# Optimization experiments

Measured on AMD Instinct MI355X. Metric: run time of the kernel, lower is better.

Reference implementation:

```python
import jax, jax.numpy as jnp
import numpy as np

K = 32          # init k
E = 0.003       # EMA rate e


def setup_inputs() -> dict:
    key = jax.random.key(0)
    k1, _ = jax.random.split(key)
    features = jax.random.normal(k1, (512, 6, 8192), dtype=jnp.float32)
    threshold = jnp.zeros((1,), dtype=jnp.float32)
    return {"features": features, "threshold": threshold}


def reference(features, threshold):
    batch_size, n_layers, d_features = features.shape
    batch_k = K * batch_size * n_layers
    flat = features.reshape(-1)                      # [B*L*D]
    topk_vals, topk_idxs = jax.lax.top_k(flat, batch_k)
    topk_vals = jax.nn.relu(topk_vals)
    out = jnp.zeros_like(flat).at[topk_idxs].set(topk_vals)
    out = out.reshape(batch_size, n_layers, d_features)
    min_k = jax.lax.stop_gradient(jnp.min(topk_vals))
    new_threshold = (1.0 - E) * threshold + E * min_k
    return out, new_threshold
```

## Files before the change

kernel.cpp:

```cpp
#include <hip/hip_runtime.h>
#include <stdint.h>

#define K_TOTAL   98304u
#define EMA_RATE  0.003f

#define SBINS      16384
#define SBIN_SHIFT 18
#define SAMPLE_VEC 131072
#define STARGET    8192u
#define P2_BINS    4096
#define P2_SHIFT   12
#define LCAP       1024
#define CAP2       65536u
#define EQCAP      256

#define MP_BLOCKS  3072
#define MP_UNROLL  8

__device__ __forceinline__ unsigned f2key(float x) {
    unsigned u = __float_as_uint(x);
    return (u & 0x80000000u) ? ~u : (u | 0x80000000u);
}
__device__ __forceinline__ float key2f(unsigned key) {
    unsigned u = (key & 0x80000000u) ? (key & 0x7FFFFFFFu) : ~key;
    return __uint_as_float(u);
}

__global__ __launch_bounds__(256) void sample_hist_kernel(
        const float4* __restrict__ in, unsigned* __restrict__ shist) {
    __shared__ unsigned h[SBINS];
    for (int i = threadIdx.x; i < SBINS; i += 256) h[i] = 0;
    __syncthreads();
    unsigned tid = blockIdx.x * 256 + threadIdx.x;
    unsigned nth = gridDim.x * 256;
    float4 v[4];
    #pragma unroll
    for (int u = 0; u < 4; ++u) {
        unsigned j = tid + u * nth;
        v[u] = (j < SAMPLE_VEC) ? in[j] : make_float4(0.f, 0.f, 0.f, 0.f);
    }
    #pragma unroll
    for (int u = 0; u < 4; ++u) {
        unsigned j = tid + u * nth;
        if (j < SAMPLE_VEC) {
            atomicAdd(&h[f2key(v[u].x) >> SBIN_SHIFT], 1u);
            atomicAdd(&h[f2key(v[u].y) >> SBIN_SHIFT], 1u);
            atomicAdd(&h[f2key(v[u].z) >> SBIN_SHIFT], 1u);
            atomicAdd(&h[f2key(v[u].w) >> SBIN_SHIFT], 1u);
        }
    }
    __syncthreads();
    for (int i = threadIdx.x; i < SBINS; i += 256) {
        unsigned c = h[i];
        if (c) atomicAdd(&shist[i], c);
    }
}

__global__ __launch_bounds__(1024) void sample_scan_kernel(
        const unsigned* __restrict__ shist, unsigned* __restrict__ res) {
    __shared__ unsigned psum[1024];
    const int T = 1024;
    const int GB = SBINS / T;
    int t = threadIdx.x;
    int hi = SBINS - 1 - t * GB;
    unsigned c[GB];
    #pragma unroll
    for (int j = 0; j < GB; ++j) c[j] = shist[hi - j];
    unsigned s = 0;
    #pragma unroll
    for (int j = 0; j < GB; ++j) s += c[j];
    psum[t] = s;
    __syncthreads();
    for (int off = 1; off < T; off <<= 1) {
        unsigned o = (t >= off) ? psum[t - off] : 0u;
        __syncthreads();
        psum[t] += o;
        __syncthreads();
    }
    unsigned cum = psum[t] - s;
    for (int j = 0; j < GB; ++j) {
        if (cum < STARGET && cum + c[j] >= STARGET) {
            unsigned bin = (unsigned)(hi - j);
            unsigned bb = (bin > 0) ? bin - 1 : 0;
            res[0] = bb << SBIN_SHIFT;
        }
        cum += c[j];
    }
}

__global__ __launch_bounds__(256) void main_pass_kernel(
        const float4* __restrict__ in, const unsigned* __restrict__ res,
        float* __restrict__ cval, unsigned* __restrict__ cidx,
        unsigned* __restrict__ gcnt, unsigned cap, int nvec) {
    __shared__ float    lval[LCAP];
    __shared__ unsigned lidx[LCAP];
    __shared__ unsigned lcnt, lbase;
    if (threadIdx.x == 0) lcnt = 0;
    __syncthreads();
    unsigned base = res[0];
    unsigned tid = blockIdx.x * 256 + threadIdx.x;
    unsigned nth = gridDim.x * 256;
    for (unsigned i0 = tid; i0 < (unsigned)nvec; i0 += MP_UNROLL * nth) {
        float4 v[MP_UNROLL];
        #pragma unroll
        for (int u = 0; u < MP_UNROLL; ++u) {
            unsigned j = i0 + u * nth;
            v[u] = (j < (unsigned)nvec) ? in[j]
                   : make_float4(-1e30f, -1e30f, -1e30f, -1e30f);
        }
        #pragma unroll
        for (int u = 0; u < MP_UNROLL; ++u) {
            unsigned j = i0 + u * nth;
            unsigned idx = 4u * j;
            float xs[4] = {v[u].x, v[u].y, v[u].z, v[u].w};
            #pragma unroll
            for (int c = 0; c < 4; ++c) {
                unsigned key = f2key(xs[c]);
                if (key >= base) {
                    unsigned p = atomicAdd(&lcnt, 1u);
                    if (p < LCAP) { lval[p] = xs[c]; lidx[p] = idx + c; }
                    else {
                        unsigned q = atomicAdd(gcnt, 1u);
                        if (q < cap) { cval[q] = xs[c]; cidx[q] = idx + c; }
                    }
                }
            }
        }
    }
    __syncthreads();
    unsigned n = min(lcnt, (unsigned)LCAP);
    if (threadIdx.x == 0) lbase = atomicAdd(gcnt, n);
    __syncthreads();
    for (unsigned j = threadIdx.x; j < n; j += 256) {
        unsigned p = lbase + j;
        if (p < cap) { cval[p] = lval[j]; cidx[p] = lidx[j]; }
    }
}

__global__ __launch_bounds__(256) void cand_hist_kernel(
        const float* __restrict__ cval, const unsigned* __restrict__ gcnt,
        const unsigned* __restrict__ res, unsigned* __restrict__ ghist,
        unsigned cap) {
    __shared__ unsigned h[P2_BINS];
    for (int i = threadIdx.x; i < P2_BINS; i += 256) h[i] = 0;
    __syncthreads();
    unsigned nc = min(*gcnt, cap);
    unsigned base = res[0];
    unsigned tid = blockIdx.x * 256 + threadIdx.x;
    unsigned nth = gridDim.x * 256;
    for (unsigned i0 = tid; i0 < nc; i0 += 4 * nth) {
        float v[4];
        #pragma unroll
        for (int u = 0; u < 4; ++u) {
            unsigned j = i0 + u * nth;
            v[u] = (j < nc) ? cval[j] : -1e30f;
        }
        #pragma unroll
        for (int u = 0; u < 4; ++u) {
            unsigned j = i0 + u * nth;
            if (j < nc) {
                unsigned g = (f2key(v[u]) - base) >> P2_SHIFT;
                if (g > P2_BINS - 1) g = P2_BINS - 1;
                atomicAdd(&h[g], 1u);
            }
        }
    }
    __syncthreads();
    for (int i = threadIdx.x; i < P2_BINS; i += 256) {
        unsigned c = h[i];
        if (c) atomicAdd(&ghist[i], c);
    }
}

__global__ __launch_bounds__(1024) void find_g_kernel(
        const unsigned* __restrict__ ghist, unsigned* __restrict__ res2) {
    __shared__ unsigned psum[1024];
    const int T = 1024;
    const int GB = P2_BINS / T;
    int t = threadIdx.x;
    int hi = P2_BINS - 1 - t * GB;
    unsigned c[GB];
    #pragma unroll
    for (int j = 0; j < GB; ++j) c[j] = ghist[hi - j];
    unsigned s = 0;
    #pragma unroll
    for (int j = 0; j < GB; ++j) s += c[j];
    psum[t] = s;
    __syncthreads();
    for (int off = 1; off < T; off <<= 1) {
        unsigned o = (t >= off) ? psum[t - off] : 0u;
        __syncthreads();
        psum[t] += o;
        __syncthreads();
    }
    unsigned cum = psum[t] - s;
    for (int j = 0; j < GB; ++j) {
        if (cum < K_TOTAL && cum + c[j] >= K_TOTAL) {
            res2[0] = (unsigned)(hi - j);
            res2[1] = K_TOTAL - cum;
        }
        cum += c[j];
    }
}

__global__ __launch_bounds__(256) void scatter_kernel(
        const float* __restrict__ cval, const unsigned* __restrict__ cidx,
        const unsigned* __restrict__ gcnt, const unsigned* __restrict__ res,
        const unsigned* __restrict__ res2,
        float* __restrict__ cval2, unsigned* __restrict__ cidx2,
        unsigned* __restrict__ cnt2, unsigned cap,
        float* __restrict__ out) {
    unsigned nc = min(*gcnt, cap);
    unsigned base = res[0];
    unsigned gstar = res2[0];
    unsigned tid = blockIdx.x * 256 + threadIdx.x;
    unsigned nth = gridDim.x * 256;
    for (unsigned i0 = tid; i0 < nc; i0 += 4 * nth) {
        float v[4];
        #pragma unroll
        for (int u = 0; u < 4; ++u) {
            unsigned j = i0 + u * nth;
            v[u] = (j < nc) ? cval[j] : -1e30f;
        }
        #pragma unroll
        for (int u = 0; u < 4; ++u) {
            unsigned j = i0 + u * nth;
            if (j < nc) {
                unsigned g = (f2key(v[u]) - base) >> P2_SHIFT;
                if (g > P2_BINS - 1) g = P2_BINS - 1;
                if (g > gstar) {
                    out[cidx[j]] = fmaxf(v[u], 0.0f);
                } else if (g == gstar) {
                    unsigned p = atomicAdd(cnt2, 1u);
                    if (p < CAP2) { cval2[p] = v[u]; cidx2[p] = cidx[j]; }
                }
            }
        }
    }
}

__global__ __launch_bounds__(256) void final_kernel(
        const float* __restrict__ cval2, const unsigned* __restrict__ cidx2,
        const unsigned* __restrict__ cnt2,
        const unsigned* __restrict__ res, const unsigned* __restrict__ res2,
        float* __restrict__ out,
        const float* __restrict__ thr_in, float* __restrict__ thr_out) {
    __shared__ unsigned h[1 << P2_SHIFT];
    __shared__ unsigned psum[256];
    __shared__ unsigned eqidx[EQCAP];
    __shared__ unsigned eqcnt;
    __shared__ unsigned sh_low, sh_need3;
    const int NB = 1 << P2_SHIFT;
    int t = threadIdx.x;
    unsigned nc2   = min(*cnt2, CAP2);
    unsigned base3 = res[0] + (res2[0] << P2_SHIFT);
    unsigned need2 = res2[1];

    for (int i = t; i < NB; i += 256) h[i] = 0;
    if (t == 0) eqcnt = 0;
    __syncthreads();
    for (unsigned i = t; i < nc2; i += 256) {
        unsigned low = f2key(cval2[i]) - base3;
        if (low > (unsigned)(NB - 1)) low = NB - 1;
        atomicAdd(&h[low], 1u);
    }
    __syncthreads();

    const int GB = NB / 256;
    int hi = NB - 1 - t * GB;
    unsigned s = 0;
    for (int j = 0; j < GB; ++j) s += h[hi - j];
    psum[t] = s;
    __syncthreads();
    for (int off = 1; off < 256; off <<= 1) {
        unsigned o = (t >= off) ? psum[t - off] : 0u;
        __syncthreads();
        psum[t] += o;
        __syncthreads();
    }
    unsigned cum = psum[t] - s;
    for (int j = 0; j < GB; ++j) {
        unsigned c = h[hi - j];
        if (cum < need2 && cum + c >= need2) {
            sh_low = (unsigned)(hi - j);
            sh_need3 = need2 - cum;
        }
        cum += c;
    }
    __syncthreads();
    unsigned kth_key = base3 + sh_low;
    unsigned need3   = sh_need3;

    for (unsigned i = t; i < nc2; i += 256) {
        float x = cval2[i];
        unsigned key = f2key(x);
        if (key > kth_key) {
            out[cidx2[i]] = fmaxf(x, 0.0f);
        } else if (key == kth_key) {
            unsigned p = atomicAdd(&eqcnt, 1u);
            if (p < EQCAP) eqidx[p] = cidx2[i];
        }
    }
    __syncthreads();

    unsigned ne = min(eqcnt, (unsigned)EQCAP);
    float vv = key2f(kth_key);
    for (unsigned e = t; e < ne; e += 256) {
        unsigned my = eqidx[e];
        unsigned rank = 0;
        for (unsigned f = 0; f < ne; ++f) rank += (eqidx[f] < my) ? 1u : 0u;
        if (rank < need3) out[my] = fmaxf(vv, 0.0f);
    }

    if (t == 0) {
        float mink = fmaxf(vv, 0.0f);
        thr_out[0] = (1.0f - EMA_RATE) * thr_in[0] + EMA_RATE * mink;
    }
}

extern "C" void kernel_launch(void* const* d_in, const int* in_sizes, int n_in,
                              void* d_out, int out_size, void* d_ws, size_t ws_size,
                              hipStream_t stream) {
    const float* feat   = (const float*)d_in[0];
    const float* thr_in = (const float*)d_in[1];
    float* out = (float*)d_out;
    int N    = in_sizes[0];
    int nvec = N / 4;

    uint8_t* w = (uint8_t*)d_ws;
    unsigned* shist = (unsigned*)w;
    unsigned* ghist = (unsigned*)(w + (64 << 10));
    unsigned* ctr   = (unsigned*)(w + (80 << 10));
    unsigned* gcnt  = ctr + 0;
    unsigned* cnt2  = ctr + 1;
    unsigned* res   = ctr + 4;
    unsigned* res2  = ctr + 8;

    size_t cand_off = (size_t)1 << 20;
    size_t avail    = (ws_size > cand_off + (CAP2 * 8 + 4096))
                        ? (ws_size - cand_off - CAP2 * 8 - 4096) / 8 : 0;
    unsigned cap = (unsigned)((avail < (size_t)(4u << 20)) ? avail : (size_t)(4u << 20));
    float*    cval  = (float*)(w + cand_off);
    unsigned* cidx  = (unsigned*)(w + cand_off + (size_t)cap * 4);
    float*    cval2 = (float*)(w + cand_off + (size_t)cap * 8);
    unsigned* cidx2 = (unsigned*)(w + cand_off + (size_t)cap * 8 + CAP2 * 4);

    hipMemsetAsync(d_ws, 0, (80 << 10) + 64, stream);
    hipMemsetAsync(d_out, 0, (size_t)N * 4, stream);

    sample_hist_kernel<<<128, 256, 0, stream>>>((const float4*)feat, shist);
    sample_scan_kernel<<<1,  1024, 0, stream>>>(shist, res);
    main_pass_kernel  <<<MP_BLOCKS, 256, 0, stream>>>((const float4*)feat, res,
                                                      cval, cidx, gcnt, cap, nvec);
    cand_hist_kernel  <<<128, 256, 0, stream>>>(cval, gcnt, res, ghist, cap);
    find_g_kernel     <<<1,  1024, 0, stream>>>(ghist, res2);
    scatter_kernel    <<<128, 256, 0, stream>>>(cval, cidx, gcnt, res, res2,
                                                cval2, cidx2, cnt2, cap, out);
    final_kernel      <<<1,   256, 0, stream>>>(cval2, cidx2, cnt2, res, res2,
                                                out, thr_in, out + N);
}
```

Measured before the change: 238.9 us.

## Fuse scans and candidate histogram into passes, zero output inside main pass

Merges the sample-scan step into the sample histogram kernel and the candidate histogram plus bin search into the main pass, each using a last-block-done counter. The main pass now also writes zeros to the output with nontemporal stores, which replaces the separate output memset. This removes three kernel launches, one full extra write pass over the output and a re-read of the candidates. In exchange, the main pass issues global histogram atomics for every candidate, and LCAP and the block count are reduced.

```diff
diff --git a/kernel.cpp b/kernel.cpp
--- a/kernel.cpp
+++ b/kernel.cpp
@@ -8,14 +8,17 @@
 #define SBIN_SHIFT 18
 #define SAMPLE_VEC 131072
 #define STARGET    8192u
+#define SMP_BLOCKS 128
+
 #define P2_BINS    4096
 #define P2_SHIFT   12
-#define LCAP       1024
+#define LCAP       512
 #define CAP2       65536u
 #define EQCAP      256
 
-#define MP_BLOCKS  3072
-#define MP_UNROLL  8
+#define MP_BLOCKS  2048
+
+typedef float v4f __attribute__((ext_vector_type(4)));
 
 __device__ __forceinline__ unsigned f2key(float x) {
     unsigned u = __float_as_uint(x);
@@ -26,52 +29,50 @@
     return __uint_as_float(u);
 }
 
-__global__ __launch_bounds__(256) void sample_hist_kernel(
-        const float4* __restrict__ in, unsigned* __restrict__ shist) {
+__global__ __launch_bounds__(256) void sample_kernel(
+        const float4* __restrict__ in, unsigned* __restrict__ shist,
+        unsigned* __restrict__ done, unsigned* __restrict__ res) {
     __shared__ unsigned h[SBINS];
-    for (int i = threadIdx.x; i < SBINS; i += 256) h[i] = 0;
-    __syncthreads();
-    unsigned tid = blockIdx.x * 256 + threadIdx.x;
+    __shared__ unsigned psum[256];
+    __shared__ unsigned lastS;
+    int t = threadIdx.x;
+    for (int i = t; i < SBINS; i += 256) h[i] = 0;
+    __syncthreads();
+    unsigned tid = blockIdx.x * 256 + t;
     unsigned nth = gridDim.x * 256;
     float4 v[4];
     #pragma unroll
-    for (int u = 0; u < 4; ++u) {
-        unsigned j = tid + u * nth;
-        v[u] = (j < SAMPLE_VEC) ? in[j] : make_float4(0.f, 0.f, 0.f, 0.f);
-    }
+    for (int u = 0; u < 4; ++u) v[u] = in[tid + u * nth];
     #pragma unroll
     for (int u = 0; u < 4; ++u) {
-        unsigned j = tid + u * nth;
-        if (j < SAMPLE_VEC) {
-            atomicAdd(&h[f2key(v[u].x) >> SBIN_SHIFT], 1u);
-            atomicAdd(&h[f2key(v[u].y) >> SBIN_SHIFT], 1u);
-            atomicAdd(&h[f2key(v[u].z) >> SBIN_SHIFT], 1u);
-            atomicAdd(&h[f2key(v[u].w) >> SBIN_SHIFT], 1u);
-        }
-    }
-    __syncthreads();
-    for (int i = threadIdx.x; i < SBINS; i += 256) {
+        atomicAdd(&h[f2key(v[u].x) >> SBIN_SHIFT], 1u);
+        atomicAdd(&h[f2key(v[u].y) >> SBIN_SHIFT], 1u);
+        atomicAdd(&h[f2key(v[u].z) >> SBIN_SHIFT], 1u);
+        atomicAdd(&h[f2key(v[u].w) >> SBIN_SHIFT], 1u);
+    }
+    __syncthreads();
+    for (int i = t; i < SBINS; i += 256) {
         unsigned c = h[i];
         if (c) atomicAdd(&shist[i], c);
     }
-}
-
-__global__ __launch_bounds__(1024) void sample_scan_kernel(
-        const unsigned* __restrict__ shist, unsigned* __restrict__ res) {
-    __shared__ unsigned psum[1024];
-    const int T = 1024;
-    const int GB = SBINS / T;
-    int t = threadIdx.x;
+    __threadfence();
+    __syncthreads();
+    if (t == 0) {
+        unsigned d = atomicAdd(done, 1u);
+        lastS = (d == gridDim.x - 1) ? 1u : 0u;
+    }
+    __syncthreads();
+    if (!lastS) return;
+
+    for (int i = t; i < SBINS; i += 256) h[i] = atomicAdd(&shist[i], 0u);
+    __syncthreads();
+    const int GB = SBINS / 256;
     int hi = SBINS - 1 - t * GB;
-    unsigned c[GB];
-    #pragma unroll
-    for (int j = 0; j < GB; ++j) c[j] = shist[hi - j];
     unsigned s = 0;
-    #pragma unroll
-    for (int j = 0; j < GB; ++j) s += c[j];
+    for (int j = 0; j < GB; ++j) s += h[hi - j];
     psum[t] = s;
     __syncthreads();
-    for (int off = 1; off < T; off <<= 1) {
+    for (int off = 1; off < 256; off <<= 1) {
         unsigned o = (t >= off) ? psum[t - off] : 0u;
         __syncthreads();
         psum[t] += o;
@@ -79,115 +80,104 @@
     }
     unsigned cum = psum[t] - s;
     for (int j = 0; j < GB; ++j) {
-        if (cum < STARGET && cum + c[j] >= STARGET) {
+        unsigned c = h[hi - j];
+        if (cum < STARGET && cum + c >= STARGET) {
             unsigned bin = (unsigned)(hi - j);
             unsigned bb = (bin > 0) ? bin - 1 : 0;
             res[0] = bb << SBIN_SHIFT;
         }
-        cum += c[j];
-    }
-}
-
-__global__ __launch_bounds__(256) void main_pass_kernel(
-        const float4* __restrict__ in, const unsigned* __restrict__ res,
+        cum += c;
+    }
+}
+
+#define PROCESS_VEC(vv, jvec)                                                \
+    {                                                                        \
+        unsigned idx0_ = 4u * (jvec);                                        \
+        float xs_[4] = {(vv).x, (vv).y, (vv).z, (vv).w};                     \
+        _Pragma("unroll")                                                    \
+        for (int c_ = 0; c_ < 4; ++c_) {                                     \
+            unsigned key_ = f2key(xs_[c_]);                                  \
+            if (key_ >= base) {                             \
+                unsigned g_ = (key_ - base) >> P2_SHIFT;                     \
+                if (g_ > P2_BINS - 1) g_ = P2_BINS - 1;                      \
+                atomicAdd(&ghist[g_], 1u);                                   \
+                unsigned p_ = atomicAdd(&lcnt, 1u);                          \
+                if (p_ < LCAP) {                                             \
+                    ((float*)ubuf)[p_] = xs_[c_];                            \
+                    ubuf[LCAP + p_] = idx0_ + (unsigned)c_;                  \
+                } else {                              \
+                    unsigned q_ = atomicAdd(gcnt, 1u);                       \
+                    if (q_ < cap) { cval[q_] = xs_[c_]; cidx[q_] = idx0_ + (unsigned)c_; } \
+                }                                                            \
+            }                                                                \
+        }                                                                    \
+    }
+
+__global__ __launch_bounds__(256, 8) void main_pass_kernel(
+        const float4* __restrict__ in, float4* __restrict__ outv,
+        const unsigned* __restrict__ res,
         float* __restrict__ cval, unsigned* __restrict__ cidx,
-        unsigned* __restrict__ gcnt, unsigned cap, int nvec) {
-    __shared__ float    lval[LCAP];
-    __shared__ unsigned lidx[LCAP];
-    __shared__ unsigned lcnt, lbase;
-    if (threadIdx.x == 0) lcnt = 0;
+        unsigned* __restrict__ gcnt, unsigned* __restrict__ ghist,
+        unsigned* __restrict__ done, unsigned* __restrict__ res2,
+        unsigned cap, unsigned nvec) {
+    __shared__ unsigned ubuf[P2_BINS];
+    __shared__ unsigned psum[256];
+    __shared__ unsigned lcnt, lbase, lastS;
+    int t = threadIdx.x;
+    if (t == 0) lcnt = 0;
     __syncthreads();
     unsigned base = res[0];
-    unsigned tid = blockIdx.x * 256 + threadIdx.x;
+    unsigned tid = blockIdx.x * 256 + t;
     unsigned nth = gridDim.x * 256;
-    for (unsigned i0 = tid; i0 < (unsigned)nvec; i0 += MP_UNROLL * nth) {
-        float4 v[MP_UNROLL];
-        #pragma unroll
-        for (int u = 0; u < MP_UNROLL; ++u) {
-            unsigned j = i0 + u * nth;
-            v[u] = (j < (unsigned)nvec) ? in[j]
-                   : make_float4(-1e30f, -1e30f, -1e30f, -1e30f);
-        }
-        #pragma unroll
-        for (int u = 0; u < MP_UNROLL; ++u) {
-            unsigned j = i0 + u * nth;
-            unsigned idx = 4u * j;
-            float xs[4] = {v[u].x, v[u].y, v[u].z, v[u].w};
-            #pragma unroll
-            for (int c = 0; c < 4; ++c) {
-                unsigned key = f2key(xs[c]);
-                if (key >= base) {
-                    unsigned p = atomicAdd(&lcnt, 1u);
-                    if (p < LCAP) { lval[p] = xs[c]; lidx[p] = idx + c; }
-                    else {
-                        unsigned q = atomicAdd(gcnt, 1u);
-                        if (q < cap) { cval[q] = xs[c]; cidx[q] = idx + c; }
-                    }
-                }
-            }
-        }
-    }
+    const v4f z4 = {0.f, 0.f, 0.f, 0.f};
+
+    unsigned i0 = tid;
+    unsigned nb = nvec / (4u * nth);
+    for (unsigned b = 0; b < nb; ++b) {
+        float4 v[4];
+        #pragma unroll
+        for (int u = 0; u < 4; ++u) v[u] = in[i0 + u * nth];
+        #pragma unroll
+        for (int u = 0; u < 4; ++u)
+            __builtin_nontemporal_store(z4, (v4f*)(outv + (i0 + u * nth)));
+        #pragma unroll
+        for (int u = 0; u < 4; ++u) PROCESS_VEC(v[u], i0 + u * nth);
+        i0 += 4u * nth;
+    }
+    for (; i0 < nvec; i0 += nth) {
+        float4 v = in[i0];
+        __builtin_nontemporal_store(z4, (v4f*)(outv + i0));
+        PROCESS_VEC(v, i0);
+    }
+
     __syncthreads();
     unsigned n = min(lcnt, (unsigned)LCAP);
-    if (threadIdx.x == 0) lbase = atomicAdd(gcnt, n);
-    __syncthreads();
-    for (unsigned j = threadIdx.x; j < n; j += 256) {
+    if (t == 0) lbase = atomicAdd(gcnt, n);
+    __syncthreads();
+    for (unsigned j = t; j < n; j += 256) {
         unsigned p = lbase + j;
-        if (p < cap) { cval[p] = lval[j]; cidx[p] = lidx[j]; }
-    }
-}
-
-__global__ __launch_bounds__(256) void cand_hist_kernel(
-        const float* __restrict__ cval, const unsigned* __restrict__ gcnt,
-        const unsigned* __restrict__ res, unsigned* __restrict__ ghist,
-        unsigned cap) {
-    __shared__ unsigned h[P2_BINS];
-    for (int i = threadIdx.x; i < P2_BINS; i += 256) h[i] = 0;
-    __syncthreads();
-    unsigned nc = min(*gcnt, cap);
-    unsigned base = res[0];
-    unsigned tid = blockIdx.x * 256 + threadIdx.x;
-    unsigned nth = gridDim.x * 256;
-    for (unsigned i0 = tid; i0 < nc; i0 += 4 * nth) {
-        float v[4];
-        #pragma unroll
-        for (int u = 0; u < 4; ++u) {
-            unsigned j = i0 + u * nth;
-            v[u] = (j < nc) ? cval[j] : -1e30f;
-        }
-        #pragma unroll
-        for (int u = 0; u < 4; ++u) {
-            unsigned j = i0 + u * nth;
-            if (j < nc) {
-                unsigned g = (f2key(v[u]) - base) >> P2_SHIFT;
-                if (g > P2_BINS - 1) g = P2_BINS - 1;
-                atomicAdd(&h[g], 1u);
-            }
-        }
-    }
-    __syncthreads();
-    for (int i = threadIdx.x; i < P2_BINS; i += 256) {
-        unsigned c = h[i];
-        if (c) atomicAdd(&ghist[i], c);
-    }
-}
-
-__global__ __launch_bounds__(1024) void find_g_kernel(
-        const unsigned* __restrict__ ghist, unsigned* __restrict__ res2) {
-    __shared__ unsigned psum[1024];
-    const int T = 1024;
-    const int GB = P2_BINS / T;
-    int t = threadIdx.x;
+        if (p < cap) { cval[p] = ((float*)ubuf)[j]; cidx[p] = ubuf[LCAP + j]; }
+    }
+
+    __threadfence();
+    __syncthreads();
+    if (t == 0) {
+        unsigned d = atomicAdd(done, 1u);
+        lastS = (d == gridDim.x - 1) ? 1u : 0u;
+    }
+    __syncthreads();
+    if (!lastS) return;
+
+    for (int i = t; i < P2_BINS; i += 256) ubuf[i] = atomicAdd(&ghist[i], 0u);
+    __syncthreads();
+    const int GB = P2_BINS / 256;
     int hi = P2_BINS - 1 - t * GB;
-    unsigned c[GB];
-    #pragma unroll
-    for (int j = 0; j < GB; ++j) c[j] = ghist[hi - j];
     unsigned s = 0;
     #pragma unroll
-    for (int j = 0; j < GB; ++j) s += c[j];
+    for (int j = 0; j < GB; ++j) s += ubuf[hi - j];
     psum[t] = s;
     __syncthreads();
-    for (int off = 1; off < T; off <<= 1) {
+    for (int off = 1; off < 256; off <<= 1) {
         unsigned o = (t >= off) ? psum[t - off] : 0u;
         __syncthreads();
         psum[t] += o;
@@ -195,11 +185,12 @@
     }
     unsigned cum = psum[t] - s;
     for (int j = 0; j < GB; ++j) {
-        if (cum < K_TOTAL && cum + c[j] >= K_TOTAL) {
+        unsigned c = ubuf[hi - j];
+        if (cum < K_TOTAL && cum + c >= K_TOTAL) {
             res2[0] = (unsigned)(hi - j);
             res2[1] = K_TOTAL - cum;
         }
-        cum += c[j];
+        cum += c;
     }
 }
 
@@ -333,6 +324,8 @@
     unsigned* ctr   = (unsigned*)(w + (80 << 10));
     unsigned* gcnt  = ctr + 0;
     unsigned* cnt2  = ctr + 1;
+    unsigned* done1 = ctr + 2;
+    unsigned* done2 = ctr + 3;
     unsigned* res   = ctr + 4;
     unsigned* res2  = ctr + 8;
 
@@ -346,16 +339,16 @@
     unsigned* cidx2 = (unsigned*)(w + cand_off + (size_t)cap * 8 + CAP2 * 4);
 
     hipMemsetAsync(d_ws, 0, (80 << 10) + 64, stream);
-    hipMemsetAsync(d_out, 0, (size_t)N * 4, stream);
-
-    sample_hist_kernel<<<128, 256, 0, stream>>>((const float4*)feat, shist);
-    sample_scan_kernel<<<1,  1024, 0, stream>>>(shist, res);
-    main_pass_kernel  <<<MP_BLOCKS, 256, 0, stream>>>((const float4*)feat, res,
-                                                      cval, cidx, gcnt, cap, nvec);
-    cand_hist_kernel  <<<128, 256, 0, stream>>>(cval, gcnt, res, ghist, cap);
-    find_g_kernel     <<<1,  1024, 0, stream>>>(ghist, res2);
-    scatter_kernel    <<<128, 256, 0, stream>>>(cval, cidx, gcnt, res, res2,
-                                                cval2, cidx2, cnt2, cap, out);
-    final_kernel      <<<1,   256, 0, stream>>>(cval2, cidx2, cnt2, res, res2,
-                                                out, thr_in, out + N);
-}
+
+    sample_kernel   <<<SMP_BLOCKS, 256, 0, stream>>>((const float4*)feat,
+                                                     shist, done1, res);
+    main_pass_kernel<<<MP_BLOCKS, 256, 0, stream>>>((const float4*)feat,
+                                                    (float4*)out, res,
+                                                    cval, cidx, gcnt, ghist,
+                                                    done2, res2, cap,
+                                                    (unsigned)nvec);
+    scatter_kernel  <<<128, 256, 0, stream>>>(cval, cidx, gcnt, res, res2,
+                                              cval2, cidx2, cnt2, cap, out);
+    final_kernel    <<<1,   256, 0, stream>>>(cval2, cidx2, cnt2, res, res2,
+                                              out, thr_in, out + N);
+}
```

Measured after the change: 666.0 us. 179% more time.

## Fuse output zeroing, sample histogram and scan into one kernel

Applied to the files above, without the earlier changes.

Replaces the output memset plus the separate sample-histogram and single-block scan kernels with one kernel. Every block zeroes a slice of the output, the first 128 blocks also build the sample histogram, and the last block to finish (found with an atomic counter) runs the threshold scan. The main pass also moves from 3072 to 2048 blocks and from a guarded 8-wide unroll to an unguarded 6-wide batch with a scalar tail. The aim is to cut launch count and serialization, at the cost of a last-block-done pattern that relies on threadfence and atomics for correctness.

```diff
diff --git a/kernel.cpp b/kernel.cpp
--- a/kernel.cpp
+++ b/kernel.cpp
@@ -8,14 +8,18 @@
 #define SBIN_SHIFT 18
 #define SAMPLE_VEC 131072
 #define STARGET    8192u
+#define SMP_BLOCKS 128
+
 #define P2_BINS    4096
 #define P2_SHIFT   12
 #define LCAP       1024
 #define CAP2       65536u
 #define EQCAP      256
 
-#define MP_BLOCKS  3072
-#define MP_UNROLL  8
+#define FILL_BLOCKS 512
+#define FILL_PT     48
+#define MP_BLOCKS   2048
+#define MP_BATCH    6
 
 __device__ __forceinline__ unsigned f2key(float x) {
     unsigned u = __float_as_uint(x);
@@ -26,52 +30,67 @@
     return __uint_as_float(u);
 }
 
-__global__ __launch_bounds__(256) void sample_hist_kernel(
-        const float4* __restrict__ in, unsigned* __restrict__ shist) {
+__global__ __launch_bounds__(256) void fill_sample_kernel(
+        const float4* __restrict__ in, float4* __restrict__ outv,
+        unsigned* __restrict__ shist, unsigned* __restrict__ done,
+        unsigned* __restrict__ res, unsigned nvec) {
     __shared__ unsigned h[SBINS];
-    for (int i = threadIdx.x; i < SBINS; i += 256) h[i] = 0;
-    __syncthreads();
-    unsigned tid = blockIdx.x * 256 + threadIdx.x;
-    unsigned nth = gridDim.x * 256;
-    float4 v[4];
+    __shared__ unsigned psum[256];
+    __shared__ unsigned lastS;
+    int t = threadIdx.x;
+    bool sampler = (blockIdx.x < SMP_BLOCKS);
+
+    if (sampler) {
+        for (int i = t; i < SBINS; i += 256) h[i] = 0;
+        __syncthreads();
+    }
+
+    const float4 z4 = make_float4(0.f, 0.f, 0.f, 0.f);
+    unsigned slice = blockIdx.x * (256u * FILL_PT);
     #pragma unroll
-    for (int u = 0; u < 4; ++u) {
-        unsigned j = tid + u * nth;
-        v[u] = (j < SAMPLE_VEC) ? in[j] : make_float4(0.f, 0.f, 0.f, 0.f);
-    }
-    #pragma unroll
-    for (int u = 0; u < 4; ++u) {
-        unsigned j = tid + u * nth;
-        if (j < SAMPLE_VEC) {
+    for (int k = 0; k < FILL_PT; ++k) {
+        unsigned j = slice + (unsigned)k * 256u + (unsigned)t;
+        if (j < nvec) outv[j] = z4;
+    }
+
+    if (sampler) {
+        unsigned tid = blockIdx.x * 256 + t;
+        unsigned snth = SMP_BLOCKS * 256;
+        float4 v[4];
+        #pragma unroll
+        for (int u = 0; u < 4; ++u) v[u] = in[tid + u * snth];
+        #pragma unroll
+        for (int u = 0; u < 4; ++u) {
             atomicAdd(&h[f2key(v[u].x) >> SBIN_SHIFT], 1u);
             atomicAdd(&h[f2key(v[u].y) >> SBIN_SHIFT], 1u);
             atomicAdd(&h[f2key(v[u].z) >> SBIN_SHIFT], 1u);
             atomicAdd(&h[f2key(v[u].w) >> SBIN_SHIFT], 1u);
         }
-    }
-    __syncthreads();
-    for (int i = threadIdx.x; i < SBINS; i += 256) {
-        unsigned c = h[i];
-        if (c) atomicAdd(&shist[i], c);
-    }
-}
-
-__global__ __launch_bounds__(1024) void sample_scan_kernel(
-        const unsigned* __restrict__ shist, unsigned* __restrict__ res) {
-    __shared__ unsigned psum[1024];
-    const int T = 1024;
-    const int GB = SBINS / T;
-    int t = threadIdx.x;
+        __syncthreads();
+        for (int i = t; i < SBINS; i += 256) {
+            unsigned c = h[i];
+            if (c) atomicAdd(&shist[i], c);
+        }
+    }
+
+    __threadfence();
+    __syncthreads();
+    if (t == 0) {
+        unsigned d = atomicAdd(done, 1u);
+        lastS = (d == gridDim.x - 1) ? 1u : 0u;
+    }
+    __syncthreads();
+    if (!lastS) return;
+
+    for (int i = t; i < SBINS; i += 256) h[i] = atomicAdd(&shist[i], 0u);
+    __syncthreads();
+    const int GB = SBINS / 256;
     int hi = SBINS - 1 - t * GB;
-    unsigned c[GB];
-    #pragma unroll
-    for (int j = 0; j < GB; ++j) c[j] = shist[hi - j];
     unsigned s = 0;
-    #pragma unroll
-    for (int j = 0; j < GB; ++j) s += c[j];
+    for (int j = 0; j < GB; ++j) s += h[hi - j];
     psum[t] = s;
     __syncthreads();
-    for (int off = 1; off < T; off <<= 1) {
+    for (int off = 1; off < 256; off <<= 1) {
         unsigned o = (t >= off) ? psum[t - off] : 0u;
         __syncthreads();
         psum[t] += o;
@@ -79,19 +98,20 @@
     }
     unsigned cum = psum[t] - s;
     for (int j = 0; j < GB; ++j) {
-        if (cum < STARGET && cum + c[j] >= STARGET) {
+        unsigned c = h[hi - j];
+        if (cum < STARGET && cum + c >= STARGET) {
             unsigned bin = (unsigned)(hi - j);
             unsigned bb = (bin > 0) ? bin - 1 : 0;
             res[0] = bb << SBIN_SHIFT;
         }
-        cum += c[j];
+        cum += c;
     }
 }
 
 __global__ __launch_bounds__(256) void main_pass_kernel(
         const float4* __restrict__ in, const unsigned* __restrict__ res,
         float* __restrict__ cval, unsigned* __restrict__ cidx,
-        unsigned* __restrict__ gcnt, unsigned cap, int nvec) {
+        unsigned* __restrict__ gcnt, unsigned cap, unsigned nvec) {
     __shared__ float    lval[LCAP];
     __shared__ unsigned lidx[LCAP];
     __shared__ unsigned lcnt, lbase;
@@ -100,16 +120,14 @@
     unsigned base = res[0];
     unsigned tid = blockIdx.x * 256 + threadIdx.x;
     unsigned nth = gridDim.x * 256;
-    for (unsigned i0 = tid; i0 < (unsigned)nvec; i0 += MP_UNROLL * nth) {
-        float4 v[MP_UNROLL];
-        #pragma unroll
-        for (int u = 0; u < MP_UNROLL; ++u) {
-            unsigned j = i0 + u * nth;
-            v[u] = (j < (unsigned)nvec) ? in[j]
-                   : make_float4(-1e30f, -1e30f, -1e30f, -1e30f);
-        }
-        #pragma unroll
-        for (int u = 0; u < MP_UNROLL; ++u) {
+    unsigned i0 = tid;
+    unsigned nb = nvec / (MP_BATCH * nth);
+    for (unsigned b = 0; b < nb; ++b) {
+        float4 v[MP_BATCH];
+        #pragma unroll
+        for (int u = 0; u < MP_BATCH; ++u) v[u] = in[i0 + u * nth];
+        #pragma unroll
+        for (int u = 0; u < MP_BATCH; ++u) {
             unsigned j = i0 + u * nth;
             unsigned idx = 4u * j;
             float xs[4] = {v[u].x, v[u].y, v[u].z, v[u].w};
@@ -123,6 +141,24 @@
                         unsigned q = atomicAdd(gcnt, 1u);
                         if (q < cap) { cval[q] = xs[c]; cidx[q] = idx + c; }
                     }
+                }
+            }
+        }
+        i0 += MP_BATCH * nth;
+    }
+    for (; i0 < nvec; i0 += nth) {
+        float4 v = in[i0];
+        unsigned idx = 4u * i0;
+        float xs[4] = {v.x, v.y, v.z, v.w};
+        #pragma unroll
+        for (int c = 0; c < 4; ++c) {
+            unsigned key = f2key(xs[c]);
+            if (key >= base) {
+                unsigned p = atomicAdd(&lcnt, 1u);
+                if (p < LCAP) { lval[p] = xs[c]; lidx[p] = idx + c; }
+                else {
+                    unsigned q = atomicAdd(gcnt, 1u);
+                    if (q < cap) { cval[q] = xs[c]; cidx[q] = idx + c; }
                 }
             }
         }
@@ -333,6 +369,7 @@
     unsigned* ctr   = (unsigned*)(w + (80 << 10));
     unsigned* gcnt  = ctr + 0;
     unsigned* cnt2  = ctr + 1;
+    unsigned* done1 = ctr + 2;
     unsigned* res   = ctr + 4;
     unsigned* res2  = ctr + 8;
 
@@ -346,12 +383,14 @@
     unsigned* cidx2 = (unsigned*)(w + cand_off + (size_t)cap * 8 + CAP2 * 4);
 
     hipMemsetAsync(d_ws, 0, (80 << 10) + 64, stream);
-    hipMemsetAsync(d_out, 0, (size_t)N * 4, stream);
-
-    sample_hist_kernel<<<128, 256, 0, stream>>>((const float4*)feat, shist);
-    sample_scan_kernel<<<1,  1024, 0, stream>>>(shist, res);
+
+    fill_sample_kernel<<<FILL_BLOCKS, 256, 0, stream>>>((const float4*)feat,
+                                                        (float4*)out, shist,
+                                                        done1, res,
+                                                        (unsigned)nvec);
     main_pass_kernel  <<<MP_BLOCKS, 256, 0, stream>>>((const float4*)feat, res,
-                                                      cval, cidx, gcnt, cap, nvec);
+                                                      cval, cidx, gcnt, cap,
+                                                      (unsigned)nvec);
     cand_hist_kernel  <<<128, 256, 0, stream>>>(cval, gcnt, res, ghist, cap);
     find_g_kernel     <<<1,  1024, 0, stream>>>(ghist, res2);
     scatter_kernel    <<<128, 256, 0, stream>>>(cval, cidx, gcnt, res, res2,
```

After: 302.5 us. 26.6% more time.
